# Performance work log

Hardware: AMD Instinct MI355X
Metric: run time of the kernel (lower is better)

Reference implementation:

```python
import jax, jax.numpy as jnp
import numpy as np

K = 128      # knowledge_n (= net1 = prednet output width)
LOW = 64     # low_dim
PP = 64      # pp_dim
STU = 50000  # student_n
EXER = 20000 # exer_n
S_RANGES = [(0, 9999), (10000, 19999)]
NR = len(S_RANGES)
B = 4096


def setup_inputs() -> dict:
    key = jax.random.key(0)
    ks = jax.random.split(key, 16)

    def xavier(k, shape):
        fan_in, fan_out = shape[-1], shape[-2] if len(shape) > 1 else shape[-1]
        lim = np.sqrt(6.0 / (fan_in + fan_out))
        return jax.random.uniform(k, shape, jnp.float32, -lim, lim)

    return {
        "stu_id": jax.random.randint(ks[0], (B,), 0, STU),
        "exer_id": jax.random.randint(ks[1], (B,), 0, EXER),
        "kn_emb": jnp.ones((B, K), jnp.float32),
        "student_emb": xavier(ks[2], (NR, STU, LOW)),          # ParameterList stacked
        "prompt_stu": xavier(ks[3], (STU, PP)),
        "knowledge_emb": jax.random.normal(ks[4], (K, LOW), jnp.float32),
        "k_difficulty": xavier(ks[5], (EXER, LOW)),
        "s_exer_vectors": jax.random.uniform(ks[6], (NR, PP), jnp.float32),
        "W1": xavier(ks[7], (K, K + LOW)),                      # prednet_full1 (no bias)
        "W2": xavier(ks[8], (K, K + LOW)),                      # prednet_full2 (no bias)
        "W3": xavier(ks[9], (1, K)),                            # prednet_full3
        "b3": jnp.zeros((1,), jnp.float32),
        "fc1_W": xavier(ks[10], (K, PP + K)),
        "fc1_b": jnp.zeros((K,), jnp.float32),
        "fc2_W": xavier(ks[11], (K, PP + K)),
        "fc2_b": jnp.zeros((K,), jnp.float32),
    }


def reference(stu_id, exer_id, kn_emb, student_emb, prompt_stu, knowledge_emb,
              k_difficulty, s_exer_vectors, W1, W2, W3, b3, fc1_W, fc1_b, fc2_W, fc2_b):
    sig = jax.nn.sigmoid
    kle = knowledge_emb  # [K, LOW]

    # --- student side ---
    # prompt_stu.repeat(NR, 1) then index_select == index prompt_stu with stu_id % STU
    p_stu = prompt_stu[stu_id % STU]                              # [B, PP]
    stu_cat = student_emb.reshape(NR * STU, LOW)                  # concat of ParameterList
    old_stu = sig(stu_cat[stu_id] @ kle.T)                        # [B, K]
    stu_e = sig(jnp.concatenate([p_stu, old_stu], 1) @ fc1_W.T + fc1_b)  # [B, K]

    # --- exercise side ---
    counts = np.array([r[1] - r[0] + 1 for r in S_RANGES])
    temp_vectors = jnp.repeat(s_exer_vectors, counts, axis=0, total_repeat_length=EXER)
    p_exer = sig(temp_vectors[exer_id])                           # [B, PP]
    old_exer = sig(sig(k_difficulty[exer_id]) @ kle.T)            # [B, K]
    exer_e = sig(jnp.concatenate([p_exer, old_exer], 1) @ fc2_W.T + fc2_b)  # [B, K]

    # --- per-concept interaction ---
    # cat([x_broadcast, kn_vector], 2) @ W.T splits into x @ Wa.T + kle @ Wb.T
    W1a, W1b = W1[:, :K], W1[:, K:]
    W2a, W2b = W2[:, :K], W2[:, K:]
    preference = sig((stu_e @ W1a.T)[:, None, :] + (kle @ W1b.T)[None, :, :])   # [B, K, K]
    diff = sig((exer_e @ W2a.T)[:, None, :] + (kle @ W2b.T)[None, :, :])        # [B, K, K]

    o = sig((preference - diff) @ W3.T + b3)                      # [B, K, 1]
    sum_out = jnp.sum(o * kn_emb[:, :, None], axis=1)             # [B, 1]
    count = jnp.sum(kn_emb, axis=1, keepdims=True)
    return sum_out / count
```

## Files before the change

### kernel.cpp

```cpp
#include <hip/hip_runtime.h>
#include <hip/hip_bf16.h>

#define STUN   50000
#define BATCH  4096
#define LOG2E  1.4426950408889634f

__device__ __forceinline__ float fexp2(float x){ return __builtin_amdgcn_exp2f(x); }
__device__ __forceinline__ float frcp (float x){ return __builtin_amdgcn_rcpf(x); }
__device__ __forceinline__ float fsig (float x){ return frcp(1.0f + fexp2(-LOG2E * x)); }

__global__ __launch_bounds__(128) void k_pre(
    const float* __restrict__ kle,
    const float* __restrict__ W1,
    const float* __restrict__ W2,
    const float* __restrict__ fc1_W,
    const float* __restrict__ fc2_W,
    float* __restrict__ kle4,
    float* __restrict__ fc1i,
    float* __restrict__ fc2i,
    float* __restrict__ W1ai,
    float* __restrict__ W2ai,
    float* __restrict__ E1i,
    float* __restrict__ E2i)
{
    const int bid = blockIdx.x;
    const int t   = threadIdx.x;
    if (bid < 16) {
        const int u4 = bid;
        float4 v;
        v.x = kle[t * 64 + u4 * 4 + 0];
        v.y = kle[t * 64 + u4 * 4 + 1];
        v.z = kle[t * 64 + u4 * 4 + 2];
        v.w = kle[t * 64 + u4 * 4 + 3];
        *(float4*)&kle4[(u4 * 128 + t) * 4] = v;
    } else if (bid < 64) {
        const int u4 = bid - 16;
        float4 v;
        v.x = fc1_W[t * 192 + u4 * 4 + 0];
        v.y = fc1_W[t * 192 + u4 * 4 + 1];
        v.z = fc1_W[t * 192 + u4 * 4 + 2];
        v.w = fc1_W[t * 192 + u4 * 4 + 3];
        *(float4*)&fc1i[(u4 * 128 + t) * 4] = v;
    } else if (bid < 112) {
        const int u4 = bid - 64;
        float4 v;
        v.x = fc2_W[t * 192 + u4 * 4 + 0];
        v.y = fc2_W[t * 192 + u4 * 4 + 1];
        v.z = fc2_W[t * 192 + u4 * 4 + 2];
        v.w = fc2_W[t * 192 + u4 * 4 + 3];
        *(float4*)&fc2i[(u4 * 128 + t) * 4] = v;
    } else if (bid < 144) {
        const int u4 = bid - 112;
        float4 v;
        v.x = W1[t * 192 + u4 * 4 + 0];
        v.y = W1[t * 192 + u4 * 4 + 1];
        v.z = W1[t * 192 + u4 * 4 + 2];
        v.w = W1[t * 192 + u4 * 4 + 3];
        *(float4*)&W1ai[(u4 * 128 + t) * 4] = v;
    } else if (bid < 176) {
        const int u4 = bid - 144;
        float4 v;
        v.x = W2[t * 192 + u4 * 4 + 0];
        v.y = W2[t * 192 + u4 * 4 + 1];
        v.z = W2[t * 192 + u4 * 4 + 2];
        v.w = W2[t * 192 + u4 * 4 + 3];
        *(float4*)&W2ai[(u4 * 128 + t) * 4] = v;
    } else if (bid < 304) {
        const int j = bid - 176;
        float acc = 0.f;
        #pragma unroll
        for (int u4 = 0; u4 < 16; ++u4) {
            const float4 kv = *(const float4*)&kle[t * 64 + u4 * 4];
            const float4 wv = *(const float4*)&W1[j * 192 + 128 + u4 * 4];
            acc += kv.x * wv.x + kv.y * wv.y + kv.z * wv.z + kv.w * wv.w;
        }
        E1i[((j >> 2) * 128 + t) * 4 + (j & 3)] = fexp2(-LOG2E * acc);
    } else {
        const int j = bid - 304;
        float acc = 0.f;
        #pragma unroll
        for (int u4 = 0; u4 < 16; ++u4) {
            const float4 kv = *(const float4*)&kle[t * 64 + u4 * 4];
            const float4 wv = *(const float4*)&W2[j * 192 + 128 + u4 * 4];
            acc += kv.x * wv.x + kv.y * wv.y + kv.z * wv.z + kv.w * wv.w;
        }
        E2i[((j >> 2) * 128 + t) * 4 + (j & 3)] = fexp2(-LOG2E * acc);
    }
}

__global__ __launch_bounds__(512, 4) void k_prep(
    const int*   __restrict__ stu_id,
    const int*   __restrict__ exer_id,
    const float* __restrict__ student_emb,
    const float* __restrict__ prompt_stu,
    const float* __restrict__ k_diff,
    const float* __restrict__ s_exer,
    const float* __restrict__ kle4,
    const float* __restrict__ fc1i,
    const float* __restrict__ fc2i,
    const float* __restrict__ W1ai,
    const float* __restrict__ W2ai,
    const float* __restrict__ fc1_b,
    const float* __restrict__ fc2_b,
    float* __restrict__ es1o,
    float* __restrict__ es2o)
{
    __shared__ __align__(16) float sh_in [4][64][8];
    __shared__ __align__(16) float sh_old[2][128][8];
    __shared__ __align__(16) float sh_e  [2][128][8];
    __shared__ __align__(16) float ps    [2][8][128];

    const int t  = threadIdx.x;
    const int b0 = blockIdx.x * 8;

    {
        const int g   = t >> 6;
        const int u   = t & 63;
        const int sid = stu_id[b0 + g];
        const int eid = exer_id[b0 + g];
        const int er  = (eid >= 10000) ? 1 : 0;
        sh_in[0][u][g] = student_emb[sid * 64 + u];
        sh_in[1][u][g] = fsig(k_diff[eid * 64 + u]);
        sh_in[2][u][g] = prompt_stu[(sid % STUN) * 64 + u];
        sh_in[3][u][g] = fsig(s_exer[er * 64 + u]);
    }
    __syncthreads();

    const int ug   = t >> 8;
    const int tt   = t & 255;
    const int half = tt >> 7;
    const int idx  = tt & 127;

    float acc[8];

#define FMA8(xbase) { \
        const float4 x0 = *(const float4*)&(xbase)[0]; \
        const float4 x1 = *(const float4*)&(xbase)[4]; \
        acc[0] += wv * x0.x; acc[1] += wv * x0.y; acc[2] += wv * x0.z; acc[3] += wv * x0.w; \
        acc[4] += wv * x1.x; acc[5] += wv * x1.y; acc[6] += wv * x1.z; acc[7] += wv * x1.w; }

#define WSTEP(WARR, XARR, u4) { \
        const float4 w4 = *(const float4*)&WARR[((u4) * 128 + idx) * 4]; \
        { const float wv = w4.x; FMA8(XARR[(u4)*4+0]); } \
        { const float wv = w4.y; FMA8(XARR[(u4)*4+1]); } \
        { const float wv = w4.z; FMA8(XARR[(u4)*4+2]); } \
        { const float wv = w4.w; FMA8(XARR[(u4)*4+3]); } }

#define WSTEPO(WARR, XARR, u4, uoff) { \
        const float4 w4 = *(const float4*)&WARR[((u4) * 128 + idx) * 4]; \
        { const float wv = w4.x; FMA8(XARR[((u4)-(uoff))*4+0]); } \
        { const float wv = w4.y; FMA8(XARR[((u4)-(uoff))*4+1]); } \
        { const float wv = w4.z; FMA8(XARR[((u4)-(uoff))*4+2]); } \
        { const float wv = w4.w; FMA8(XARR[((u4)-(uoff))*4+3]); } }

    #pragma unroll
    for (int b = 0; b < 8; ++b) acc[b] = 0.f;
    {
        const int u4a = ug * 8;
        #pragma unroll 4
        for (int u4 = u4a; u4 < u4a + 8; ++u4) WSTEP(kle4, sh_in[half], u4);
    }
    if (ug == 1) {
        #pragma unroll
        for (int b = 0; b < 8; ++b) ps[half][b][idx] = acc[b];
    }
    __syncthreads();
    if (ug == 0) {
        #pragma unroll
        for (int b = 0; b < 8; ++b)
            sh_old[half][idx][b] = fsig(acc[b] + ps[half][b][idx]);
    }
    __syncthreads();

    #pragma unroll
    for (int b = 0; b < 8; ++b) acc[b] = 0.f;
    {
        const float* fcT = half ? fc2i : fc1i;
        if (ug == 0) {
            #pragma unroll 4
            for (int u4 = 0; u4 < 16; ++u4) WSTEP(fcT, sh_in[2 + half], u4);
            #pragma unroll 4
            for (int u4 = 16; u4 < 24; ++u4) WSTEPO(fcT, sh_old[half], u4, 16);
        } else {
            #pragma unroll 4
            for (int u4 = 24; u4 < 48; ++u4) WSTEPO(fcT, sh_old[half], u4, 16);
        }
    }
    if (ug == 1) {
        #pragma unroll
        for (int b = 0; b < 8; ++b) ps[half][b][idx] = acc[b];
    }
    __syncthreads();
    if (ug == 0) {
        const float bias = (half ? fc2_b : fc1_b)[idx];
        #pragma unroll
        for (int b = 0; b < 8; ++b)
            sh_e[half][idx][b] = fsig(acc[b] + ps[half][b][idx] + bias);
    }
    __syncthreads();

    #pragma unroll
    for (int b = 0; b < 8; ++b) acc[b] = 0.f;
    {
        const float* WT = half ? W2ai : W1ai;
        const int u4a = ug * 16;
        #pragma unroll 4
        for (int u4 = u4a; u4 < u4a + 16; ++u4) WSTEP(WT, sh_e[half], u4);
    }
    if (ug == 1) {
        #pragma unroll
        for (int b = 0; b < 8; ++b) ps[half][b][idx] = acc[b];
    }
    __syncthreads();
    if (ug == 0) {
        float* eso = half ? es2o : es1o;
        #pragma unroll
        for (int b = 0; b < 8; ++b)
            eso[(b0 + b) * 128 + idx] = fexp2(-LOG2E * (acc[b] + ps[half][b][idx]));
    }
#undef FMA8
#undef WSTEP
#undef WSTEPO
}

__global__ __launch_bounds__(256, 6) void k_main(
    const float* __restrict__ es1o,
    const float* __restrict__ es2o,
    const float* __restrict__ E1i,
    const float* __restrict__ E2i,
    const float* __restrict__ W3,
    const float* __restrict__ b3,
    const float* __restrict__ kn,
    float* __restrict__ out)
{
    __shared__ __align__(16) float ses[2][2][128];
    __shared__ float sW3[128];
    __shared__ __align__(16) float redj[2][64][2];
    __shared__ float red2_o[2][2];
    __shared__ float red2_k[2][2];

    const int t   = threadIdx.x;
    const int b0  = blockIdx.x * 2;

    if (t < 128) {
        const int row  = t >> 5;
        const int col4 = (t & 31) * 4;
        const float* src = (row < 2) ? es1o : es2o;
        *(float4*)&ses[row >> 1][row & 1][col4] =
            *(const float4*)&src[(b0 + (row & 1)) * 128 + col4];
    } else if (t < 160) {
        const int q = t - 128;
        *(float4*)&sW3[q * 4] = *(const float4*)&W3[q * 4];
    }
    __syncthreads();

    const int w   = t >> 6;
    const int kk  = t & 63;
    const int kh  = w & 1;
    const int jh  = w >> 1;
    const int k2  = kh * 64 + kk;

    const float4* E1v = (const float4*)E1i;
    const float4* E2v = (const float4*)E2i;

    float acc0 = 0.f, acc1 = 0.f;

#define COMP(acc, esv1, esv2, e1c, e2c, w3c) { \
        const float uu = (esv1) * (e1c); \
        const float vv = (esv2) * (e2c); \
        const float dd = frcp((1.f + uu) * (1.f + vv)); \
        acc += ((vv - uu) * dd) * (w3c); }

    #pragma unroll 4
    for (int j4 = 0; j4 < 16; ++j4) {
        const int jj4 = jh * 16 + j4;
        const int j   = jj4 * 4;
        const float4 e1  = E1v[jj4 * 128 + k2];
        const float4 e2  = E2v[jj4 * 128 + k2];
        const float4 w3  = *(const float4*)&sW3[j];
        const float4 s1a = *(const float4*)&ses[0][0][j];
        const float4 s1b = *(const float4*)&ses[0][1][j];
        const float4 s2a = *(const float4*)&ses[1][0][j];
        const float4 s2b = *(const float4*)&ses[1][1][j];

        COMP(acc0, s1a.x, s2a.x, e1.x, e2.x, w3.x);
        COMP(acc0, s1a.y, s2a.y, e1.y, e2.y, w3.y);
        COMP(acc0, s1a.z, s2a.z, e1.z, e2.z, w3.z);
        COMP(acc0, s1a.w, s2a.w, e1.w, e2.w, w3.w);
        COMP(acc1, s1b.x, s2b.x, e1.x, e2.x, w3.x);
        COMP(acc1, s1b.y, s2b.y, e1.y, e2.y, w3.y);
        COMP(acc1, s1b.z, s2b.z, e1.z, e2.z, w3.z);
        COMP(acc1, s1b.w, s2b.w, e1.w, e2.w, w3.w);
    }
#undef COMP

    if (jh == 1) {
        redj[kh][kk][0] = acc0;
        redj[kh][kk][1] = acc1;
    }
    __syncthreads();
    if (jh == 0) {
        const float bb3 = b3[0];
        const float t0 = acc0 + redj[kh][kk][0];
        const float t1 = acc1 + redj[kh][kk][1];
        const float o0 = fsig(t0 + bb3);
        const float o1 = fsig(t1 + bb3);
        const float kn0 = kn[(b0 + 0) * 128 + k2];
        const float kn1 = kn[(b0 + 1) * 128 + k2];
        float co0 = o0 * kn0, ck0 = kn0;
        float co1 = o1 * kn1, ck1 = kn1;
        #pragma unroll
        for (int off = 1; off < 64; off <<= 1) {
            co0 += __shfl_xor(co0, off);
            ck0 += __shfl_xor(ck0, off);
            co1 += __shfl_xor(co1, off);
            ck1 += __shfl_xor(ck1, off);
        }
        if (kk == 0) {
            red2_o[kh][0] = co0; red2_o[kh][1] = co1;
            red2_k[kh][0] = ck0; red2_k[kh][1] = ck1;
        }
    }
    __syncthreads();
    if (t < 2) {
        const float so = red2_o[0][t] + red2_o[1][t];
        const float sk = red2_k[0][t] + red2_k[1][t];
        out[b0 + t] = so / sk;
    }
}

extern "C" void kernel_launch(void* const* d_in, const int* in_sizes, int n_in,
                              void* d_out, int out_size, void* d_ws, size_t ws_size,
                              hipStream_t stream)
{
    const int*   stu_id      = (const int*)  d_in[0];
    const int*   exer_id     = (const int*)  d_in[1];
    const float* kn_emb      = (const float*)d_in[2];
    const float* student_emb = (const float*)d_in[3];
    const float* prompt_stu  = (const float*)d_in[4];
    const float* kle         = (const float*)d_in[5];
    const float* k_diff      = (const float*)d_in[6];
    const float* s_exer      = (const float*)d_in[7];
    const float* W1          = (const float*)d_in[8];
    const float* W2          = (const float*)d_in[9];
    const float* W3          = (const float*)d_in[10];
    const float* b3          = (const float*)d_in[11];
    const float* fc1_W       = (const float*)d_in[12];
    const float* fc1_b       = (const float*)d_in[13];
    const float* fc2_W       = (const float*)d_in[14];
    const float* fc2_b       = (const float*)d_in[15];
    float* out = (float*)d_out;

    float* ws   = (float*)d_ws;
    float* kle4 = ws;
    float* fc1i = kle4 + 8192;
    float* fc2i = fc1i + 24576;
    float* W1ai = fc2i + 24576;
    float* W2ai = W1ai + 16384;
    float* E1i  = W2ai + 16384;
    float* E2i  = E1i  + 16384;
    float* es1o = E2i  + 16384;
    float* es2o = es1o + BATCH * 128;

    k_pre<<<432, 128, 0, stream>>>(kle, W1, W2, fc1_W, fc2_W,
                                   kle4, fc1i, fc2i, W1ai, W2ai, E1i, E2i);
    k_prep<<<BATCH / 8, 512, 0, stream>>>(stu_id, exer_id, student_emb, prompt_stu,
                                          k_diff, s_exer, kle4, fc1i, fc2i,
                                          W1ai, W2ai, fc1_b, fc2_b, es1o, es2o);
    k_main<<<BATCH / 2, 256, 0, stream>>>(es1o, es2o, E1i, E2i, W3, b3, kn_emb, out);
}
```

Measured before the change: 51.54 us.

## Restructure k_main to loop full j range per thread, drop LDS staging

k_main now gives each thread one k column and the full 128-wide j loop for two batch rows, with 4 rows per block. The split-j reduction through shared memory and the LDS staging of es/W3 are gone, and the es, W3 vectors are read straight from global (uniform, cached) memory. k_prep writes both es vectors interleaved per row into one buffer so each row's data sits together. This removes syncs and LDS traffic at the cost of longer per-thread loops, fewer blocks and a lower occupancy hint.

```diff
diff --git a/kernel.cpp b/kernel.cpp
--- a/kernel.cpp
+++ b/kernel.cpp
@@ -102,8 +102,7 @@
     const float* __restrict__ W2ai,
     const float* __restrict__ fc1_b,
     const float* __restrict__ fc2_b,
-    float* __restrict__ es1o,
-    float* __restrict__ es2o)
+    float* __restrict__ es_g)
 {
     __shared__ __align__(16) float sh_in [4][64][8];
     __shared__ __align__(16) float sh_old[2][128][8];
@@ -213,19 +212,18 @@
     }
     __syncthreads();
     if (ug == 0) {
-        float* eso = half ? es2o : es1o;
         #pragma unroll
         for (int b = 0; b < 8; ++b)
-            eso[(b0 + b) * 128 + idx] = fexp2(-LOG2E * (acc[b] + ps[half][b][idx]));
+            es_g[(b0 + b) * 256 + half * 128 + idx] =
+                fexp2(-LOG2E * (acc[b] + ps[half][b][idx]));
     }
 #undef FMA8
 #undef WSTEP
 #undef WSTEPO
 }
 
-__global__ __launch_bounds__(256, 6) void k_main(
-    const float* __restrict__ es1o,
-    const float* __restrict__ es2o,
+__global__ __launch_bounds__(256, 4) void k_main(
+    const float* __restrict__ es_g,
     const float* __restrict__ E1i,
     const float* __restrict__ E2i,
     const float* __restrict__ W3,
@@ -233,99 +231,75 @@
     const float* __restrict__ kn,
     float* __restrict__ out)
 {
-    __shared__ __align__(16) float ses[2][2][128];
-    __shared__ float sW3[128];
-    __shared__ __align__(16) float redj[2][64][2];
-    __shared__ float red2_o[2][2];
-    __shared__ float red2_k[2][2];
-
-    const int t   = threadIdx.x;
-    const int b0  = blockIdx.x * 2;
-
-    if (t < 128) {
-        const int row  = t >> 5;
-        const int col4 = (t & 31) * 4;
-        const float* src = (row < 2) ? es1o : es2o;
-        *(float4*)&ses[row >> 1][row & 1][col4] =
-            *(const float4*)&src[(b0 + (row & 1)) * 128 + col4];
-    } else if (t < 160) {
-        const int q = t - 128;
-        *(float4*)&sW3[q * 4] = *(const float4*)&W3[q * 4];
-    }
-    __syncthreads();
-
-    const int w   = t >> 6;
-    const int kk  = t & 63;
-    const int kh  = w & 1;
-    const int jh  = w >> 1;
-    const int k2  = kh * 64 + kk;
-
-    const float4* E1v = (const float4*)E1i;
-    const float4* E2v = (const float4*)E2i;
+    __shared__ float r[4][2][2];
+
+    const int t  = threadIdx.x;
+    const int b0 = blockIdx.x * 4;
+    const int k  = t & 127;
+    const int bh = t >> 7;
+    const int ba = b0 + bh * 2;
+
+    const float4* E1v = (const float4*)E1i + k;
+    const float4* E2v = (const float4*)E2i + k;
+    const float* s1a = es_g + (ba + 0) * 256;
+    const float* s2a = s1a + 128;
+    const float* s1b = es_g + (ba + 1) * 256;
+    const float* s2b = s1b + 128;
 
     float acc0 = 0.f, acc1 = 0.f;
 
-#define COMP(acc, esv1, esv2, e1c, e2c, w3c) { \
-        const float uu = (esv1) * (e1c); \
-        const float vv = (esv2) * (e2c); \
+#define COMP(acc, s1c, s2c, e1c, e2c, w3c) { \
+        const float uu = (s1c) * (e1c); \
+        const float vv = (s2c) * (e2c); \
         const float dd = frcp((1.f + uu) * (1.f + vv)); \
-        acc += ((vv - uu) * dd) * (w3c); }
+        acc = fmaf((vv - uu) * dd, (w3c), acc); }
 
     #pragma unroll 4
-    for (int j4 = 0; j4 < 16; ++j4) {
-        const int jj4 = jh * 16 + j4;
-        const int j   = jj4 * 4;
-        const float4 e1  = E1v[jj4 * 128 + k2];
-        const float4 e2  = E2v[jj4 * 128 + k2];
-        const float4 w3  = *(const float4*)&sW3[j];
-        const float4 s1a = *(const float4*)&ses[0][0][j];
-        const float4 s1b = *(const float4*)&ses[0][1][j];
-        const float4 s2a = *(const float4*)&ses[1][0][j];
-        const float4 s2b = *(const float4*)&ses[1][1][j];
-
-        COMP(acc0, s1a.x, s2a.x, e1.x, e2.x, w3.x);
-        COMP(acc0, s1a.y, s2a.y, e1.y, e2.y, w3.y);
-        COMP(acc0, s1a.z, s2a.z, e1.z, e2.z, w3.z);
-        COMP(acc0, s1a.w, s2a.w, e1.w, e2.w, w3.w);
-        COMP(acc1, s1b.x, s2b.x, e1.x, e2.x, w3.x);
-        COMP(acc1, s1b.y, s2b.y, e1.y, e2.y, w3.y);
-        COMP(acc1, s1b.z, s2b.z, e1.z, e2.z, w3.z);
-        COMP(acc1, s1b.w, s2b.w, e1.w, e2.w, w3.w);
+    for (int j4 = 0; j4 < 32; ++j4) {
+        const float4 e1  = E1v[j4 * 128];
+        const float4 e2  = E2v[j4 * 128];
+        const float4 w3  = *(const float4*)&W3[j4 * 4];
+        const float4 p1a = *(const float4*)&s1a[j4 * 4];
+        const float4 p2a = *(const float4*)&s2a[j4 * 4];
+        const float4 p1b = *(const float4*)&s1b[j4 * 4];
+        const float4 p2b = *(const float4*)&s2b[j4 * 4];
+        COMP(acc0, p1a.x, p2a.x, e1.x, e2.x, w3.x);
+        COMP(acc0, p1a.y, p2a.y, e1.y, e2.y, w3.y);
+        COMP(acc0, p1a.z, p2a.z, e1.z, e2.z, w3.z);
+        COMP(acc0, p1a.w, p2a.w, e1.w, e2.w, w3.w);
+        COMP(acc1, p1b.x, p2b.x, e1.x, e2.x, w3.x);
+        COMP(acc1, p1b.y, p2b.y, e1.y, e2.y, w3.y);
+        COMP(acc1, p1b.z, p2b.z, e1.z, e2.z, w3.z);
+        COMP(acc1, p1b.w, p2b.w, e1.w, e2.w, w3.w);
     }
 #undef COMP
 
-    if (jh == 1) {
-        redj[kh][kk][0] = acc0;
-        redj[kh][kk][1] = acc1;
-    }
-    __syncthreads();
-    if (jh == 0) {
-        const float bb3 = b3[0];
-        const float t0 = acc0 + redj[kh][kk][0];
-        const float t1 = acc1 + redj[kh][kk][1];
-        const float o0 = fsig(t0 + bb3);
-        const float o1 = fsig(t1 + bb3);
-        const float kn0 = kn[(b0 + 0) * 128 + k2];
-        const float kn1 = kn[(b0 + 1) * 128 + k2];
-        float co0 = o0 * kn0, ck0 = kn0;
-        float co1 = o1 * kn1, ck1 = kn1;
-        #pragma unroll
-        for (int off = 1; off < 64; off <<= 1) {
-            co0 += __shfl_xor(co0, off);
-            ck0 += __shfl_xor(ck0, off);
-            co1 += __shfl_xor(co1, off);
-            ck1 += __shfl_xor(ck1, off);
-        }
-        if (kk == 0) {
-            red2_o[kh][0] = co0; red2_o[kh][1] = co1;
-            red2_k[kh][0] = ck0; red2_k[kh][1] = ck1;
-        }
-    }
-    __syncthreads();
-    if (t < 2) {
-        const float so = red2_o[0][t] + red2_o[1][t];
-        const float sk = red2_k[0][t] + red2_k[1][t];
-        out[b0 + t] = so / sk;
+    const float bb3 = b3[0];
+    const float o0  = fsig(acc0 + bb3);
+    const float o1  = fsig(acc1 + bb3);
+    const float kn0 = kn[(ba + 0) * 128 + k];
+    const float kn1 = kn[(ba + 1) * 128 + k];
+    float co0 = o0 * kn0, ck0 = kn0;
+    float co1 = o1 * kn1, ck1 = kn1;
+    #pragma unroll
+    for (int off = 1; off < 64; off <<= 1) {
+        co0 += __shfl_xor(co0, off);
+        ck0 += __shfl_xor(ck0, off);
+        co1 += __shfl_xor(co1, off);
+        ck1 += __shfl_xor(ck1, off);
+    }
+    const int w = t >> 6;
+    if ((t & 63) == 0) {
+        r[w][0][0] = co0; r[w][0][1] = ck0;
+        r[w][1][0] = co1; r[w][1][1] = ck1;
+    }
+    __syncthreads();
+    if (t < 4) {
+        const int pair = t >> 1;
+        const int i    = t & 1;
+        const float so = r[pair * 2][i][0] + r[pair * 2 + 1][i][0];
+        const float sk = r[pair * 2][i][1] + r[pair * 2 + 1][i][1];
+        out[b0 + pair * 2 + i] = so / sk;
     }
 }
 
@@ -359,13 +333,12 @@
     float* W2ai = W1ai + 16384;
     float* E1i  = W2ai + 16384;
     float* E2i  = E1i  + 16384;
-    float* es1o = E2i  + 16384;
-    float* es2o = es1o + BATCH * 128;
-
-    k_pre<<<432, 128, 0, stream>>>(kle, W1, W2, fc1_W, fc2_W,
-                                   kle4, fc1i, fc2i, W1ai, W2ai, E1i, E2i);
+    float* es_g = E2i  + 16384;
+
+    k_pre <<<432, 128, 0, stream>>>(kle, W1, W2, fc1_W, fc2_W,
+                                    kle4, fc1i, fc2i, W1ai, W2ai, E1i, E2i);
     k_prep<<<BATCH / 8, 512, 0, stream>>>(stu_id, exer_id, student_emb, prompt_stu,
                                           k_diff, s_exer, kle4, fc1i, fc2i,
-                                          W1ai, W2ai, fc1_b, fc2_b, es1o, es2o);
-    k_main<<<BATCH / 2, 256, 0, stream>>>(es1o, es2o, E1i, E2i, W3, b3, kn_emb, out);
+                                          W1ai, W2ai, fc1_b, fc2_b, es_g);
+    k_main<<<BATCH / 4, 256, 0, stream>>>(es_g, E1i, E2i, W3, b3, kn_emb, out);
 }
```

New measurement: 58.43 us. 1.13x slower.

## Restructure prep GEMVs to 4x8 register tiles with split-K partial reduction

Applied to the files above, without the earlier changes.

The prep kernel now uses 256 threads instead of 512. Each thread computes 4 output columns by 8 batch rows, reading plain transposed weights (kleT, fc1T, etc.) as float4 along the output dimension. Each of the four waves takes a K-slice, and the partial sums are combined through a padded shared-memory buffer. The intent is better register reuse of the weight and activation loads and fewer threads competing for work. The cost is a four-way shared-memory reduction and more register pressure, with occupancy hinted at 2 blocks. The pre-transpose kernel now writes scalar transposed layouts across 960 blocks.

```diff
diff --git a/kernel.cpp b/kernel.cpp
--- a/kernel.cpp
+++ b/kernel.cpp
@@ -15,58 +15,33 @@
     const float* __restrict__ W2,
     const float* __restrict__ fc1_W,
     const float* __restrict__ fc2_W,
-    float* __restrict__ kle4,
-    float* __restrict__ fc1i,
-    float* __restrict__ fc2i,
-    float* __restrict__ W1ai,
-    float* __restrict__ W2ai,
+    float* __restrict__ kleT,
+    float* __restrict__ fc1T,
+    float* __restrict__ fc2T,
+    float* __restrict__ W1aT,
+    float* __restrict__ W2aT,
     float* __restrict__ E1i,
     float* __restrict__ E2i)
 {
     const int bid = blockIdx.x;
     const int t   = threadIdx.x;
-    if (bid < 16) {
-        const int u4 = bid;
-        float4 v;
-        v.x = kle[t * 64 + u4 * 4 + 0];
-        v.y = kle[t * 64 + u4 * 4 + 1];
-        v.z = kle[t * 64 + u4 * 4 + 2];
-        v.w = kle[t * 64 + u4 * 4 + 3];
-        *(float4*)&kle4[(u4 * 128 + t) * 4] = v;
-    } else if (bid < 64) {
-        const int u4 = bid - 16;
-        float4 v;
-        v.x = fc1_W[t * 192 + u4 * 4 + 0];
-        v.y = fc1_W[t * 192 + u4 * 4 + 1];
-        v.z = fc1_W[t * 192 + u4 * 4 + 2];
-        v.w = fc1_W[t * 192 + u4 * 4 + 3];
-        *(float4*)&fc1i[(u4 * 128 + t) * 4] = v;
-    } else if (bid < 112) {
-        const int u4 = bid - 64;
-        float4 v;
-        v.x = fc2_W[t * 192 + u4 * 4 + 0];
-        v.y = fc2_W[t * 192 + u4 * 4 + 1];
-        v.z = fc2_W[t * 192 + u4 * 4 + 2];
-        v.w = fc2_W[t * 192 + u4 * 4 + 3];
-        *(float4*)&fc2i[(u4 * 128 + t) * 4] = v;
-    } else if (bid < 144) {
-        const int u4 = bid - 112;
-        float4 v;
-        v.x = W1[t * 192 + u4 * 4 + 0];
-        v.y = W1[t * 192 + u4 * 4 + 1];
-        v.z = W1[t * 192 + u4 * 4 + 2];
-        v.w = W1[t * 192 + u4 * 4 + 3];
-        *(float4*)&W1ai[(u4 * 128 + t) * 4] = v;
-    } else if (bid < 176) {
-        const int u4 = bid - 144;
-        float4 v;
-        v.x = W2[t * 192 + u4 * 4 + 0];
-        v.y = W2[t * 192 + u4 * 4 + 1];
-        v.z = W2[t * 192 + u4 * 4 + 2];
-        v.w = W2[t * 192 + u4 * 4 + 3];
-        *(float4*)&W2ai[(u4 * 128 + t) * 4] = v;
-    } else if (bid < 304) {
-        const int j = bid - 176;
+    if (bid < 64) {
+        const int u = bid;
+        kleT[u * 128 + t] = kle[t * 64 + u];
+    } else if (bid < 256) {
+        const int u = bid - 64;
+        fc1T[u * 128 + t] = fc1_W[t * 192 + u];
+    } else if (bid < 448) {
+        const int u = bid - 256;
+        fc2T[u * 128 + t] = fc2_W[t * 192 + u];
+    } else if (bid < 576) {
+        const int u = bid - 448;
+        W1aT[u * 128 + t] = W1[t * 192 + u];
+    } else if (bid < 704) {
+        const int u = bid - 576;
+        W2aT[u * 128 + t] = W2[t * 192 + u];
+    } else if (bid < 832) {
+        const int j = bid - 704;
         float acc = 0.f;
         #pragma unroll
         for (int u4 = 0; u4 < 16; ++u4) {
@@ -76,7 +51,7 @@
         }
         E1i[((j >> 2) * 128 + t) * 4 + (j & 3)] = fexp2(-LOG2E * acc);
     } else {
-        const int j = bid - 304;
+        const int j = bid - 832;
         float acc = 0.f;
         #pragma unroll
         for (int u4 = 0; u4 < 16; ++u4) {
@@ -88,139 +63,145 @@
     }
 }
 
-__global__ __launch_bounds__(512, 4) void k_prep(
+__global__ __launch_bounds__(256, 2) void k_prep(
     const int*   __restrict__ stu_id,
     const int*   __restrict__ exer_id,
     const float* __restrict__ student_emb,
     const float* __restrict__ prompt_stu,
     const float* __restrict__ k_diff,
     const float* __restrict__ s_exer,
-    const float* __restrict__ kle4,
-    const float* __restrict__ fc1i,
-    const float* __restrict__ fc2i,
-    const float* __restrict__ W1ai,
-    const float* __restrict__ W2ai,
+    const float* __restrict__ kleT,
+    const float* __restrict__ fc1T,
+    const float* __restrict__ fc2T,
+    const float* __restrict__ W1aT,
+    const float* __restrict__ W2aT,
     const float* __restrict__ fc1_b,
     const float* __restrict__ fc2_b,
     float* __restrict__ es1o,
     float* __restrict__ es2o)
 {
     __shared__ __align__(16) float sh_in [4][64][8];
-    __shared__ __align__(16) float sh_old[2][128][8];
-    __shared__ __align__(16) float sh_e  [2][128][8];
-    __shared__ __align__(16) float ps    [2][8][128];
+    __shared__ __align__(16) float sh_old[2][128][12];
+    __shared__ __align__(16) float sh_e  [2][128][12];
+    __shared__ __align__(16) float ps[4][2][32][36];
 
     const int t  = threadIdx.x;
     const int b0 = blockIdx.x * 8;
 
     {
-        const int g   = t >> 6;
-        const int u   = t & 63;
+        const int g   = t >> 5;
+        const int l   = t & 31;
         const int sid = stu_id[b0 + g];
         const int eid = exer_id[b0 + g];
         const int er  = (eid >= 10000) ? 1 : 0;
-        sh_in[0][u][g] = student_emb[sid * 64 + u];
-        sh_in[1][u][g] = fsig(k_diff[eid * 64 + u]);
-        sh_in[2][u][g] = prompt_stu[(sid % STUN) * 64 + u];
-        sh_in[3][u][g] = fsig(s_exer[er * 64 + u]);
-    }
-    __syncthreads();
-
-    const int ug   = t >> 8;
-    const int tt   = t & 255;
-    const int half = tt >> 7;
-    const int idx  = tt & 127;
-
-    float acc[8];
-
-#define FMA8(xbase) { \
-        const float4 x0 = *(const float4*)&(xbase)[0]; \
-        const float4 x1 = *(const float4*)&(xbase)[4]; \
-        acc[0] += wv * x0.x; acc[1] += wv * x0.y; acc[2] += wv * x0.z; acc[3] += wv * x0.w; \
-        acc[4] += wv * x1.x; acc[5] += wv * x1.y; acc[6] += wv * x1.z; acc[7] += wv * x1.w; }
-
-#define WSTEP(WARR, XARR, u4) { \
-        const float4 w4 = *(const float4*)&WARR[((u4) * 128 + idx) * 4]; \
-        { const float wv = w4.x; FMA8(XARR[(u4)*4+0]); } \
-        { const float wv = w4.y; FMA8(XARR[(u4)*4+1]); } \
-        { const float wv = w4.z; FMA8(XARR[(u4)*4+2]); } \
-        { const float wv = w4.w; FMA8(XARR[(u4)*4+3]); } }
-
-#define WSTEPO(WARR, XARR, u4, uoff) { \
-        const float4 w4 = *(const float4*)&WARR[((u4) * 128 + idx) * 4]; \
-        { const float wv = w4.x; FMA8(XARR[((u4)-(uoff))*4+0]); } \
-        { const float wv = w4.y; FMA8(XARR[((u4)-(uoff))*4+1]); } \
-        { const float wv = w4.z; FMA8(XARR[((u4)-(uoff))*4+2]); } \
-        { const float wv = w4.w; FMA8(XARR[((u4)-(uoff))*4+3]); } }
-
-    #pragma unroll
-    for (int b = 0; b < 8; ++b) acc[b] = 0.f;
-    {
-        const int u4a = ug * 8;
+        #pragma unroll
+        for (int it = 0; it < 2; ++it) {
+            const int u = l + 32 * it;
+            sh_in[0][u][g] = student_emb[sid * 64 + u];
+            sh_in[1][u][g] = fsig(k_diff[eid * 64 + u]);
+            sh_in[2][u][g] = prompt_stu[(sid % STUN) * 64 + u];
+            sh_in[3][u][g] = fsig(s_exer[er * 64 + u]);
+        }
+    }
+    __syncthreads();
+
+    const int wv   = t >> 6;
+    const int l    = t & 63;
+    const int half = l >> 5;
+    const int iq   = l & 31;
+    float* myps = &ps[wv][half][iq][0];
+
+    const int ch   = t >> 7;
+    const int cidx = t & 127;
+    const int ciq  = cidx >> 2;
+    const int cc   = cidx & 3;
+
+    float a[4][8];
+
+#define CLR { _Pragma("unroll") for (int c = 0; c < 4; ++c) \
+              _Pragma("unroll") for (int b = 0; b < 8; ++b) a[c][b] = 0.f; }
+
+#define FMAC(c, wc) { \
+    a[c][0] = fmaf(wc, x0.x, a[c][0]); a[c][1] = fmaf(wc, x0.y, a[c][1]); \
+    a[c][2] = fmaf(wc, x0.z, a[c][2]); a[c][3] = fmaf(wc, x0.w, a[c][3]); \
+    a[c][4] = fmaf(wc, x1.x, a[c][4]); a[c][5] = fmaf(wc, x1.y, a[c][5]); \
+    a[c][6] = fmaf(wc, x1.z, a[c][6]); a[c][7] = fmaf(wc, x1.w, a[c][7]); }
+
+#define GSTEP(wp, xp) { \
+    const float4 w4 = *(const float4*)(wp); \
+    const float4 x0 = *(const float4*)&(xp)[0]; \
+    const float4 x1 = *(const float4*)&(xp)[4]; \
+    FMAC(0, w4.x); FMAC(1, w4.y); FMAC(2, w4.z); FMAC(3, w4.w); }
+
+#define PSTORE { _Pragma("unroll") for (int b = 0; b < 8; ++b) \
+    *(float4*)&myps[b * 4] = make_float4(a[0][b], a[1][b], a[2][b], a[3][b]); }
+
+#define PCOMB(res) float res[8]; \
+    _Pragma("unroll") for (int b = 0; b < 8; ++b) \
+        res[b] = ps[0][ch][ciq][b * 4 + cc] + ps[1][ch][ciq][b * 4 + cc] \
+               + ps[2][ch][ciq][b * 4 + cc] + ps[3][ch][ciq][b * 4 + cc];
+
+    CLR;
+    {
+        const int u0 = wv * 16;
         #pragma unroll 4
-        for (int u4 = u4a; u4 < u4a + 8; ++u4) WSTEP(kle4, sh_in[half], u4);
-    }
-    if (ug == 1) {
-        #pragma unroll
-        for (int b = 0; b < 8; ++b) ps[half][b][idx] = acc[b];
-    }
-    __syncthreads();
-    if (ug == 0) {
+        for (int u = u0; u < u0 + 16; ++u)
+            GSTEP(&kleT[u * 128 + iq * 4], sh_in[half][u]);
+    }
+    PSTORE;
+    __syncthreads();
+    {
+        PCOMB(s);
+        #pragma unroll
+        for (int b = 0; b < 8; ++b) sh_old[ch][cidx][b] = fsig(s[b]);
+    }
+    __syncthreads();
+
+    CLR;
+    {
+        const float* fcT = half ? fc2T : fc1T;
+        const int u0 = wv * 48;
+        const int ue_in = (u0 + 48 < 64) ? u0 + 48 : 64;
+        #pragma unroll 4
+        for (int u = u0; u < ue_in; ++u)
+            GSTEP(&fcT[u * 128 + iq * 4], sh_in[2 + half][u]);
+        const int us_old = (u0 > 64) ? u0 : 64;
+        #pragma unroll 4
+        for (int u = us_old; u < u0 + 48; ++u)
+            GSTEP(&fcT[u * 128 + iq * 4], sh_old[half][u - 64]);
+    }
+    PSTORE;
+    __syncthreads();
+    {
+        PCOMB(s);
+        const float bias = (ch ? fc2_b : fc1_b)[cidx];
+        #pragma unroll
+        for (int b = 0; b < 8; ++b) sh_e[ch][cidx][b] = fsig(s[b] + bias);
+    }
+    __syncthreads();
+
+    CLR;
+    {
+        const float* WT = half ? W2aT : W1aT;
+        const int u0 = wv * 32;
+        #pragma unroll 4
+        for (int u = u0; u < u0 + 32; ++u)
+            GSTEP(&WT[u * 128 + iq * 4], sh_e[half][u]);
+    }
+    PSTORE;
+    __syncthreads();
+    {
+        PCOMB(s);
+        float* eso = ch ? es2o : es1o;
         #pragma unroll
         for (int b = 0; b < 8; ++b)
-            sh_old[half][idx][b] = fsig(acc[b] + ps[half][b][idx]);
-    }
-    __syncthreads();
-
-    #pragma unroll
-    for (int b = 0; b < 8; ++b) acc[b] = 0.f;
-    {
-        const float* fcT = half ? fc2i : fc1i;
-        if (ug == 0) {
-            #pragma unroll 4
-            for (int u4 = 0; u4 < 16; ++u4) WSTEP(fcT, sh_in[2 + half], u4);
-            #pragma unroll 4
-            for (int u4 = 16; u4 < 24; ++u4) WSTEPO(fcT, sh_old[half], u4, 16);
-        } else {
-            #pragma unroll 4
-            for (int u4 = 24; u4 < 48; ++u4) WSTEPO(fcT, sh_old[half], u4, 16);
-        }
-    }
-    if (ug == 1) {
-        #pragma unroll
-        for (int b = 0; b < 8; ++b) ps[half][b][idx] = acc[b];
-    }
-    __syncthreads();
-    if (ug == 0) {
-        const float bias = (half ? fc2_b : fc1_b)[idx];
-        #pragma unroll
-        for (int b = 0; b < 8; ++b)
-            sh_e[half][idx][b] = fsig(acc[b] + ps[half][b][idx] + bias);
-    }
-    __syncthreads();
-
-    #pragma unroll
-    for (int b = 0; b < 8; ++b) acc[b] = 0.f;
-    {
-        const float* WT = half ? W2ai : W1ai;
-        const int u4a = ug * 16;
-        #pragma unroll 4
-        for (int u4 = u4a; u4 < u4a + 16; ++u4) WSTEP(WT, sh_e[half], u4);
-    }
-    if (ug == 1) {
-        #pragma unroll
-        for (int b = 0; b < 8; ++b) ps[half][b][idx] = acc[b];
-    }
-    __syncthreads();
-    if (ug == 0) {
-        float* eso = half ? es2o : es1o;
-        #pragma unroll
-        for (int b = 0; b < 8; ++b)
-            eso[(b0 + b) * 128 + idx] = fexp2(-LOG2E * (acc[b] + ps[half][b][idx]));
-    }
-#undef FMA8
-#undef WSTEP
-#undef WSTEPO
+            eso[(b0 + b) * 128 + cidx] = fexp2(-LOG2E * s[b]);
+    }
+#undef CLR
+#undef FMAC
+#undef GSTEP
+#undef PSTORE
+#undef PCOMB
 }
 
 __global__ __launch_bounds__(256, 6) void k_main(
@@ -352,20 +333,20 @@
     float* out = (float*)d_out;
 
     float* ws   = (float*)d_ws;
-    float* kle4 = ws;
-    float* fc1i = kle4 + 8192;
-    float* fc2i = fc1i + 24576;
-    float* W1ai = fc2i + 24576;
-    float* W2ai = W1ai + 16384;
-    float* E1i  = W2ai + 16384;
+    float* kleT = ws;
+    float* fc1T = kleT + 8192;
+    float* fc2T = fc1T + 24576;
+    float* W1aT = fc2T + 24576;
+    float* W2aT = W1aT + 16384;
+    float* E1i  = W2aT + 16384;
     float* E2i  = E1i  + 16384;
     float* es1o = E2i  + 16384;
     float* es2o = es1o + BATCH * 128;
 
-    k_pre<<<432, 128, 0, stream>>>(kle, W1, W2, fc1_W, fc2_W,
-                                   kle4, fc1i, fc2i, W1ai, W2ai, E1i, E2i);
-    k_prep<<<BATCH / 8, 512, 0, stream>>>(stu_id, exer_id, student_emb, prompt_stu,
-                                          k_diff, s_exer, kle4, fc1i, fc2i,
-                                          W1ai, W2ai, fc1_b, fc2_b, es1o, es2o);
+    k_pre <<<960, 128, 0, stream>>>(kle, W1, W2, fc1_W, fc2_W,
+                                    kleT, fc1T, fc2T, W1aT, W2aT, E1i, E2i);
+    k_prep<<<BATCH / 8, 256, 0, stream>>>(stu_id, exer_id, student_emb, prompt_stu,
+                                          k_diff, s_exer, kleT, fc1T, fc2T,
+                                          W1aT, W2aT, fc1_b, fc2_b, es1o, es2o);
     k_main<<<BATCH / 2, 256, 0, stream>>>(es1o, es2o, E1i, E2i, W3, b3, kn_emb, out);
 }
```

Result: faster. 48.03 us (-6.8%).
